# Kernel optimization log

Hardware: AMD Instinct MI355X
Metric: run time of the kernel (lower is better)

The kernel has to match this reference:

```python
import jax, jax.numpy as jnp
import numpy as np

# Config matching the torch module
NUM_HEADS = 12
NUM_FRAMES = 8
NUM_THEADS = 2
DIM = 768
HEAD_DIM = DIM // NUM_HEADS
SCALE = HEAD_DIM ** -0.5
ADAPTER_SCALE = 1.0


def setup_inputs() -> dict:
    key = jax.random.key(0)
    ks = jax.random.split(key, 6)
    BT, N, C = 64, 197, DIM  # 8 videos * 8 frames, 197 tokens
    H = int(C * 0.25)  # adapter hidden = 192
    std = 0.02
    return {
        "x": jax.random.normal(ks[0], (BT, N, C), jnp.float32),
        "a_w1": jax.random.normal(ks[1], (C, H), jnp.float32) * std,
        "a_b1": jnp.zeros((H,), jnp.float32),
        "a_w2": jax.random.normal(ks[2], (H, C), jnp.float32) * std,
        "a_b2": jnp.zeros((C,), jnp.float32),
        "qkv_w": jax.random.normal(ks[3], (C, 3 * C), jnp.float32) * std,
        "qkv_b": jnp.zeros((3 * C,), jnp.float32),
        "proj_w": jax.random.normal(ks[4], (C, C), jnp.float32) * std,
        "proj_b": jnp.zeros((C,), jnp.float32),
    }


def head_reallocation(x):
    # x: [BT, H, N, hd] -> temporal shift of first NUM_THEADS heads (from past frame)
    # and next NUM_THEADS heads (from future frame).
    bt, h, n, d = x.shape
    feat = x.reshape(bt // NUM_FRAMES, NUM_FRAMES, h, n, d)
    out = feat
    out = out.at[:, 1:, :NUM_THEADS].set(feat[:, :-1, :NUM_THEADS])
    out = out.at[:, :-1, NUM_THEADS:2 * NUM_THEADS].set(feat[:, 1:, NUM_THEADS:2 * NUM_THEADS])
    return out.reshape(bt, h, n, d)


def reference(x, a_w1, a_b1, a_w2, a_b2, qkv_w, qkv_b, proj_w, proj_b):
    B, N, C = x.shape
    # shared input adapter (skip connection, scale=1)
    xs = (x @ a_w1 + a_b1) @ a_w2 + a_b2
    x = x + xs * ADAPTER_SCALE
    # fused qkv projection -> [3, B, H, N, hd]
    qkv = (x @ qkv_w + qkv_b).reshape(B, N, 3, NUM_HEADS, HEAD_DIM)
    qkv = jnp.transpose(qkv, (2, 0, 3, 1, 4))
    q, k, v = qkv[0], qkv[1], qkv[2]
    k = head_reallocation(k)
    v = head_reallocation(v)
    attn = jnp.einsum("bhqd,bhkd->bhqk", q, k) * SCALE
    attn = jax.nn.softmax(attn, axis=-1)
    out = jnp.einsum("bhqk,bhkd->bhqd", attn, v)
    out = jnp.transpose(out, (0, 2, 1, 3)).reshape(B, N, C)
    return out @ proj_w + proj_b
```

## Files before the change

### kernel.cpp

```cpp
#include <hip/hip_runtime.h>
#include <hip/hip_bf16.h>

typedef unsigned short u16;
typedef __attribute__((ext_vector_type(8))) short bf16x8;
typedef __attribute__((ext_vector_type(8))) unsigned short u16x8;
typedef __attribute__((ext_vector_type(4))) float f32x4;

#define NBT 64
#define SEQ 197
#define CDIM 768
#define NH 12
#define HD 64
#define MVALID (NBT * SEQ)
#define MPAD 12672
#define HADP 192
#define HPAD 256
#define QKVSZ (NBT * NH * SEQ * HD)

__device__ __forceinline__ u16 f2b(float f) {
    __hip_bfloat16 h = __float2bfloat16(f);
    return __builtin_bit_cast(u16, h);
}

#define GLL16(gp, lp) __builtin_amdgcn_global_load_lds( \
    (__attribute__((address_space(1))) void*)(gp),      \
    (__attribute__((address_space(3))) void*)(lp), 16, 0, 0)

__global__ __launch_bounds__(256) void cast_x_kernel(const float* __restrict__ x, u16* __restrict__ xb) {
    long i = ((long)blockIdx.x * 256 + threadIdx.x) * 8;
    u16x8 r;
    if (i < (long)MVALID * CDIM) {
        const float4* p = (const float4*)(x + i);
        float4 a = p[0], b = p[1];
        r[0] = f2b(a.x); r[1] = f2b(a.y); r[2] = f2b(a.z); r[3] = f2b(a.w);
        r[4] = f2b(b.x); r[5] = f2b(b.y); r[6] = f2b(b.z); r[7] = f2b(b.w);
    } else {
#pragma unroll
        for (int j = 0; j < 8; ++j) r[j] = 0;
    }
    *(u16x8*)(xb + i) = r;
}

__global__ __launch_bounds__(256) void transpose_cast_kernel(
    const float* __restrict__ in, u16* __restrict__ out, int K, int N, int KP) {
    __shared__ float tile[64][65];
    int k0 = blockIdx.x * 64;
    int n0 = blockIdx.y * 64;
    int c  = threadIdx.x & 63;
    int r0 = threadIdx.x >> 6;
#pragma unroll
    for (int rr = r0; rr < 64; rr += 4) {
        int k = k0 + rr, n = n0 + c;
        tile[rr][c] = (k < K && n < N) ? in[(long)k * N + n] : 0.f;
    }
    __syncthreads();
#pragma unroll
    for (int rr = r0; rr < 64; rr += 4) {
        out[(long)(n0 + rr) * KP + k0 + c] = f2b(tile[c][rr]);
    }
}

template <int MODE, int NB>
__global__ __launch_bounds__(256, 2) void gemm_kernel(
    const u16* __restrict__ A, const u16* __restrict__ Bt,
    const float* __restrict__ bias, const float* __restrict__ resid,
    u16* __restrict__ ob, float* __restrict__ of, int K) {
    __shared__ __align__(16) u16 As[2][128 * 64];
    __shared__ __align__(16) u16 Bs[2][128 * 64];
    const int tid  = threadIdx.x;
    const int lane = tid & 63;
    const int w    = tid >> 6;
    const int wm   = w >> 1, wn = w & 1;

    const int nwg  = (int)gridDim.x;
    const int bid  = (int)blockIdx.x;
    const int q    = nwg >> 3, r = nwg & 7;
    const int xcd  = bid & 7;
    const int lid  = bid >> 3;
    const int wgid = (xcd < r ? xcd * (q + 1) : r * (q + 1) + (xcd - r) * q) + lid;
    const long m0  = (long)(wgid / NB) * 128;
    const long n0  = (long)(wgid % NB) * 128;

    const int rA = lane >> 3;
    const int cA = (lane & 7) * 8;

    const u16* ga[4];
    const u16* gb[4];
#pragma unroll
    for (int ii = 0; ii < 4; ++ii) {
        int i = w * 4 + ii;
        ga[ii] = A  + (m0 + i * 8 + rA) * K + cA;
        gb[ii] = Bt + (n0 + i * 8 + rA) * K + cA;
    }
#pragma unroll
    for (int ii = 0; ii < 4; ++ii) {
        int i = w * 4 + ii;
        GLL16(ga[ii], &As[0][i * 512]);
        GLL16(gb[ii], &Bs[0][i * 512]);
    }

    int aoff[4], boff[4];
#pragma unroll
    for (int t = 0; t < 4; ++t) {
        aoff[t] = (wm * 64 + t * 16 + (lane & 15)) * 64 + (lane >> 4) * 8;
        boff[t] = (wn * 64 + t * 16 + (lane & 15)) * 64 + (lane >> 4) * 8;
    }

    f32x4 acc[4][4] = {};
    const int kSteps = K >> 6;
    __syncthreads();
    int buf = 0;
    for (int kt = 0; kt < kSteps; ++kt) {
        if (kt + 1 < kSteps) {
#pragma unroll
            for (int ii = 0; ii < 4; ++ii) {
                int i = w * 4 + ii;
                GLL16(ga[ii] + (kt + 1) * 64, &As[buf ^ 1][i * 512]);
                GLL16(gb[ii] + (kt + 1) * 64, &Bs[buf ^ 1][i * 512]);
            }
        }
#pragma unroll
        for (int kc = 0; kc < 2; ++kc) {
            bf16x8 af[4], bg[4];
#pragma unroll
            for (int t = 0; t < 4; ++t) af[t] = *(const bf16x8*)&As[buf][aoff[t] + kc * 32];
#pragma unroll
            for (int t = 0; t < 4; ++t) bg[t] = *(const bf16x8*)&Bs[buf][boff[t] + kc * 32];
#pragma unroll
            for (int mi = 0; mi < 4; ++mi)
#pragma unroll
                for (int ni = 0; ni < 4; ++ni)
                    acc[mi][ni] = __builtin_amdgcn_mfma_f32_16x16x32_bf16(af[mi], bg[ni], acc[mi][ni], 0, 0, 0);
        }
        __syncthreads();
        buf ^= 1;
    }

    const int rb = (lane >> 4) * 4;
    const int cl = lane & 15;
#pragma unroll
    for (int mi = 0; mi < 4; ++mi) {
#pragma unroll
        for (int rr = 0; rr < 4; ++rr) {
            long m = m0 + wm * 64 + mi * 16 + rb + rr;
#pragma unroll
            for (int ni = 0; ni < 4; ++ni) {
                long n = n0 + wn * 64 + ni * 16 + cl;
                float v = acc[mi][ni][rr];
                if constexpr (MODE == 0) {
                    float bv = (n < HADP) ? bias[n] : 0.f;
                    ob[m * HPAD + n] = f2b(v + bv);
                } else if constexpr (MODE == 1) {
                    float val = 0.f;
                    if (m < MVALID) val = v + bias[n] + resid[m * CDIM + n];
                    ob[m * CDIM + n] = f2b(val);
                } else if constexpr (MODE == 2) {
                    if (m < MVALID) {
                        int mm = (int)m;
                        int bb = mm / SEQ;
                        int t  = mm - bb * SEQ;
                        int nn = (int)n;
                        int which = nn / CDIM;
                        int c  = nn - which * CDIM;
                        int hh = c >> 6, d = c & 63;
                        ob[(long)which * QKVSZ + ((long)(bb * NH + hh) * SEQ + t) * HD + d] = f2b(v + bias[nn]);
                    }
                } else {
                    if (m < MVALID) of[m * CDIM + n] = v + bias[n];
                }
            }
        }
    }
}

__global__ __launch_bounds__(256, 2) void attn_kernel(
    const u16* __restrict__ qb, const u16* __restrict__ kb, const u16* __restrict__ vb,
    u16* __restrict__ aout) {
    __shared__ __align__(16) u16 Vt[64 * 232];
    __shared__ __align__(16) u16 P[4][16 * 232];
    const int bid = blockIdx.x;
    const int b = bid / NH;
    const int h = bid - b * NH;
    const int f = b & 7;
    int fs = (h < 2) ? (f > 0 ? f - 1 : 0) : ((h < 4) ? (f < 7 ? f + 1 : 7) : f);
    const int bsrc = (b & ~7) + fs;
    const u16* Qp = qb + (long)(b    * NH + h) * SEQ * HD;
    const u16* Kp = kb + (long)(bsrc * NH + h) * SEQ * HD;
    const u16* Vp = vb + (long)(bsrc * NH + h) * SEQ * HD;

    const int tid  = threadIdx.x;
    const int lane = tid & 63;
    const int w    = tid >> 6;
    const int cl   = lane & 15;
    const int lg   = lane >> 4;

    {
        unsigned int* z1 = (unsigned int*)Vt;
        for (int i = tid; i < 64 * 232 / 2; i += 256) z1[i] = 0;
        unsigned int* z2 = (unsigned int*)&P[0][0];
        for (int i = tid; i < 4 * 16 * 232 / 2; i += 256) z2[i] = 0;
    }
    __syncthreads();
    for (int g = tid; g < SEQ * HD / 8; g += 256) {
        int t  = g >> 3;
        int d0 = (g & 7) * 8;
        u16x8 v = *(const u16x8*)(Vp + g * 8);
#pragma unroll
        for (int j = 0; j < 8; ++j) Vt[(d0 + j) * 232 + t] = v[j];
    }
    __syncthreads();

    const f32x4 vzero = {0.f, 0.f, 0.f, 0.f};
    u16* Pw = &P[w][0];
    for (int rt = w; rt < 13; rt += 4) {
        int qrow = rt * 16 + cl; if (qrow > SEQ - 1) qrow = SEQ - 1;
        bf16x8 qf0 = *(const bf16x8*)(Qp + qrow * HD + lg * 8);
        bf16x8 qf1 = *(const bf16x8*)(Qp + qrow * HD + 32 + lg * 8);
        f32x4 s[13];
#pragma unroll
        for (int ct = 0; ct < 13; ++ct) s[ct] = vzero;
#pragma unroll
        for (int ct = 0; ct < 13; ++ct) {
            int krow = ct * 16 + cl; if (krow > SEQ - 1) krow = SEQ - 1;
            bf16x8 kf0 = *(const bf16x8*)(Kp + krow * HD + lg * 8);
            bf16x8 kf1 = *(const bf16x8*)(Kp + krow * HD + 32 + lg * 8);
            s[ct] = __builtin_amdgcn_mfma_f32_16x16x32_bf16(qf0, kf0, s[ct], 0, 0, 0);
            s[ct] = __builtin_amdgcn_mfma_f32_16x16x32_bf16(qf1, kf1, s[ct], 0, 0, 0);
        }
        float rm[4] = {-1e30f, -1e30f, -1e30f, -1e30f};
#pragma unroll
        for (int ct = 0; ct < 13; ++ct) {
            bool valid = (ct * 16 + cl) <= SEQ - 1;
#pragma unroll
            for (int r = 0; r < 4; ++r) {
                float v = valid ? s[ct][r] * 0.125f : -1e30f;
                s[ct][r] = v;
                rm[r] = fmaxf(rm[r], v);
            }
        }
#pragma unroll
        for (int off = 1; off <= 8; off <<= 1)
#pragma unroll
            for (int r = 0; r < 4; ++r) rm[r] = fmaxf(rm[r], __shfl_xor(rm[r], off));
        float rs[4] = {0.f, 0.f, 0.f, 0.f};
#pragma unroll
        for (int ct = 0; ct < 13; ++ct)
#pragma unroll
            for (int r = 0; r < 4; ++r) {
                float p = __expf(s[ct][r] - rm[r]);
                s[ct][r] = p;
                rs[r] += p;
            }
#pragma unroll
        for (int off = 1; off <= 8; off <<= 1)
#pragma unroll
            for (int r = 0; r < 4; ++r) rs[r] += __shfl_xor(rs[r], off);
        float inv[4];
#pragma unroll
        for (int r = 0; r < 4; ++r) inv[r] = 1.f / rs[r];

        asm volatile("s_waitcnt lgkmcnt(0)" ::: "memory");
#pragma unroll
        for (int ct = 0; ct < 13; ++ct)
#pragma unroll
            for (int r = 0; r < 4; ++r)
                Pw[(lg * 4 + r) * 232 + ct * 16 + cl] = f2b(s[ct][r] * inv[r]);
        asm volatile("s_waitcnt lgkmcnt(0)" ::: "memory");

        bf16x8 pf[7];
#pragma unroll
        for (int ks = 0; ks < 7; ++ks)
            pf[ks] = *(const bf16x8*)(Pw + cl * 232 + ks * 32 + lg * 8);
#pragma unroll
        for (int dt = 0; dt < 4; ++dt) {
            f32x4 o = vzero;
#pragma unroll
            for (int ks = 0; ks < 7; ++ks) {
                bf16x8 vf = *(const bf16x8*)(&Vt[(dt * 16 + cl) * 232 + ks * 32 + lg * 8]);
                o = __builtin_amdgcn_mfma_f32_16x16x32_bf16(pf[ks], vf, o, 0, 0, 0);
            }
#pragma unroll
            for (int r = 0; r < 4; ++r) {
                int m = rt * 16 + lg * 4 + r;
                if (m < SEQ)
                    aout[(long)(b * SEQ + m) * CDIM + h * HD + dt * 16 + cl] = f2b(o[r]);
            }
        }
    }
}

extern "C" void kernel_launch(void* const* d_in, const int* in_sizes, int n_in,
                              void* d_out, int out_size, void* d_ws, size_t ws_size,
                              hipStream_t stream) {
    const float* x      = (const float*)d_in[0];
    const float* a_w1   = (const float*)d_in[1];
    const float* a_b1   = (const float*)d_in[2];
    const float* a_w2   = (const float*)d_in[3];
    const float* a_b2   = (const float*)d_in[4];
    const float* qkv_w  = (const float*)d_in[5];
    const float* qkv_b  = (const float*)d_in[6];
    const float* proj_w = (const float*)d_in[7];
    const float* proj_b = (const float*)d_in[8];
    float* out = (float*)d_out;
    char* ws = (char*)d_ws;

    u16* xb   = (u16*)(ws + 0);
    u16* xa   = (u16*)(ws + 19464192);
    u16* hbuf = (u16*)(ws + 38928384);
    u16* w1t  = (u16*)(ws + 45416448);
    u16* w2t  = (u16*)(ws + 45809664);
    u16* qwt  = (u16*)(ws + 46202880);
    u16* pwt  = (u16*)(ws + 49741824);
    u16* qkv  = (u16*)(ws + 50921472);
    u16* aout = xb;

    cast_x_kernel<<<4752, 256, 0, stream>>>(x, xb);
    transpose_cast_kernel<<<dim3(12, 4),  256, 0, stream>>>(a_w1,   w1t, 768, 192,  768);
    transpose_cast_kernel<<<dim3(4, 12),  256, 0, stream>>>(a_w2,   w2t, 192, 768,  256);
    transpose_cast_kernel<<<dim3(12, 36), 256, 0, stream>>>(qkv_w,  qwt, 768, 2304, 768);
    transpose_cast_kernel<<<dim3(12, 12), 256, 0, stream>>>(proj_w, pwt, 768, 768,  768);

    gemm_kernel<0, 2><<<99 * 2,  256, 0, stream>>>(xb,   w1t, a_b1,   nullptr, hbuf, nullptr, 768);
    gemm_kernel<1, 6><<<99 * 6,  256, 0, stream>>>(hbuf, w2t, a_b2,   x,       xa,   nullptr, 256);
    gemm_kernel<2, 18><<<99 * 18, 256, 0, stream>>>(xa,   qwt, qkv_b,  nullptr, qkv,  nullptr, 768);
    attn_kernel<<<NBT * NH, 256, 0, stream>>>(qkv, qkv + QKVSZ, qkv + 2 * (long)QKVSZ, aout);
    gemm_kernel<3, 6><<<99 * 6,  256, 0, stream>>>(aout, pwt, proj_b, nullptr, nullptr, out, 768);
}
```

Measured before the change: 369.7 us.

## Single-buffer GEMM LDS tiles and raise occupancy to four blocks per CU

Replaces the double-buffered LDS prefetch in the GEMM with a single buffer that is loaded, synchronised, consumed and synchronised each k-step. This halves LDS use to 32 KB per block, and launch bounds go from 2 to 4 blocks per CU so more waves can hide memory latency. The GEMM template becomes a device function wrapped by four thin kernels. In exchange, the overlap of the next tile's global load with the current tile's MFMA work within a block is lost, and the register budget per thread is tighter, which may cause spills of the 64-float accumulator.

```diff
diff --git a/kernel.cpp b/kernel.cpp
--- a/kernel.cpp
+++ b/kernel.cpp
@@ -61,12 +61,12 @@
 }
 
 template <int MODE, int NB>
-__global__ __launch_bounds__(256, 2) void gemm_kernel(
+__device__ __forceinline__ void gemm_body(
     const u16* __restrict__ A, const u16* __restrict__ Bt,
     const float* __restrict__ bias, const float* __restrict__ resid,
     u16* __restrict__ ob, float* __restrict__ of, int K) {
-    __shared__ __align__(16) u16 As[2][128 * 64];
-    __shared__ __align__(16) u16 Bs[2][128 * 64];
+    __shared__ __align__(16) u16 As[128 * 64];
+    __shared__ __align__(16) u16 Bs[128 * 64];
     const int tid  = threadIdx.x;
     const int lane = tid & 63;
     const int w    = tid >> 6;
@@ -92,12 +92,6 @@
         ga[ii] = A  + (m0 + i * 8 + rA) * K + cA;
         gb[ii] = Bt + (n0 + i * 8 + rA) * K + cA;
     }
-#pragma unroll
-    for (int ii = 0; ii < 4; ++ii) {
-        int i = w * 4 + ii;
-        GLL16(ga[ii], &As[0][i * 512]);
-        GLL16(gb[ii], &Bs[0][i * 512]);
-    }
 
     int aoff[4], boff[4];
 #pragma unroll
@@ -108,24 +102,21 @@
 
     f32x4 acc[4][4] = {};
     const int kSteps = K >> 6;
-    __syncthreads();
-    int buf = 0;
     for (int kt = 0; kt < kSteps; ++kt) {
-        if (kt + 1 < kSteps) {
-#pragma unroll
-            for (int ii = 0; ii < 4; ++ii) {
-                int i = w * 4 + ii;
-                GLL16(ga[ii] + (kt + 1) * 64, &As[buf ^ 1][i * 512]);
-                GLL16(gb[ii] + (kt + 1) * 64, &Bs[buf ^ 1][i * 512]);
-            }
-        }
+#pragma unroll
+        for (int ii = 0; ii < 4; ++ii) {
+            int i = w * 4 + ii;
+            GLL16(ga[ii] + kt * 64, &As[i * 512]);
+            GLL16(gb[ii] + kt * 64, &Bs[i * 512]);
+        }
+        __syncthreads();
 #pragma unroll
         for (int kc = 0; kc < 2; ++kc) {
             bf16x8 af[4], bg[4];
 #pragma unroll
-            for (int t = 0; t < 4; ++t) af[t] = *(const bf16x8*)&As[buf][aoff[t] + kc * 32];
-#pragma unroll
-            for (int t = 0; t < 4; ++t) bg[t] = *(const bf16x8*)&Bs[buf][boff[t] + kc * 32];
+            for (int t = 0; t < 4; ++t) af[t] = *(const bf16x8*)&As[aoff[t] + kc * 32];
+#pragma unroll
+            for (int t = 0; t < 4; ++t) bg[t] = *(const bf16x8*)&Bs[boff[t] + kc * 32];
 #pragma unroll
             for (int mi = 0; mi < 4; ++mi)
 #pragma unroll
@@ -133,7 +124,6 @@
                     acc[mi][ni] = __builtin_amdgcn_mfma_f32_16x16x32_bf16(af[mi], bg[ni], acc[mi][ni], 0, 0, 0);
         }
         __syncthreads();
-        buf ^= 1;
     }
 
     const int rb = (lane >> 4) * 4;
@@ -173,6 +163,27 @@
     }
 }
 
+__global__ __launch_bounds__(256, 4) void gemm_a1(
+    const u16* __restrict__ A, const u16* __restrict__ Bt, const float* __restrict__ bias,
+    u16* __restrict__ ob, int K) {
+    gemm_body<0, 2>(A, Bt, bias, nullptr, ob, nullptr, K);
+}
+__global__ __launch_bounds__(256, 4) void gemm_a2(
+    const u16* __restrict__ A, const u16* __restrict__ Bt, const float* __restrict__ bias,
+    const float* __restrict__ resid, u16* __restrict__ ob, int K) {
+    gemm_body<1, 6>(A, Bt, bias, resid, ob, nullptr, K);
+}
+__global__ __launch_bounds__(256, 4) void gemm_qkv(
+    const u16* __restrict__ A, const u16* __restrict__ Bt, const float* __restrict__ bias,
+    u16* __restrict__ ob, int K) {
+    gemm_body<2, 18>(A, Bt, bias, nullptr, ob, nullptr, K);
+}
+__global__ __launch_bounds__(256, 4) void gemm_proj(
+    const u16* __restrict__ A, const u16* __restrict__ Bt, const float* __restrict__ bias,
+    float* __restrict__ of, int K) {
+    gemm_body<3, 6>(A, Bt, bias, nullptr, nullptr, of, K);
+}
+
 __global__ __launch_bounds__(256, 2) void attn_kernel(
     const u16* __restrict__ qb, const u16* __restrict__ kb, const u16* __restrict__ vb,
     u16* __restrict__ aout) {
@@ -320,9 +331,9 @@
     transpose_cast_kernel<<<dim3(12, 36), 256, 0, stream>>>(qkv_w,  qwt, 768, 2304, 768);
     transpose_cast_kernel<<<dim3(12, 12), 256, 0, stream>>>(proj_w, pwt, 768, 768,  768);
 
-    gemm_kernel<0, 2><<<99 * 2,  256, 0, stream>>>(xb,   w1t, a_b1,   nullptr, hbuf, nullptr, 768);
-    gemm_kernel<1, 6><<<99 * 6,  256, 0, stream>>>(hbuf, w2t, a_b2,   x,       xa,   nullptr, 256);
-    gemm_kernel<2, 18><<<99 * 18, 256, 0, stream>>>(xa,   qwt, qkv_b,  nullptr, qkv,  nullptr, 768);
+    gemm_a1  <<<99 * 2,  256, 0, stream>>>(xb,   w1t, a_b1,  hbuf, 768);
+    gemm_a2  <<<99 * 6,  256, 0, stream>>>(hbuf, w2t, a_b2,  x, xa, 256);
+    gemm_qkv <<<99 * 18, 256, 0, stream>>>(xa,   qwt, qkv_b, qkv,   768);
     attn_kernel<<<NBT * NH, 256, 0, stream>>>(qkv, qkv + QKVSZ, qkv + 2 * (long)QKVSZ, aout);
-    gemm_kernel<3, 6><<<99 * 6,  256, 0, stream>>>(aout, pwt, proj_b, nullptr, nullptr, out, 768);
-}
+    gemm_proj<<<99 * 6,  256, 0, stream>>>(aout, pwt, proj_b, out,  768);
+}
```

After: 311.0 us. 15.9% less time.
